# Kernel tuning notes

Measured on AMD Instinct MI355X. Metric: run time of the kernel, lower is better.

## Reference

```python
import jax, jax.numpy as jnp
import numpy as np

DIM, H, DH = 1024, 16, 64
SCALE = 1.0 / np.sqrt(DH)


def setup_inputs() -> dict:
    key = jax.random.key(0)
    ks = jax.random.split(key, 16)
    B, S = 2, 2048
    glorot = jax.nn.initializers.glorot_uniform()
    def qkv(k):
        return glorot(k, (DIM, H, DH), jnp.float32)
    inp = {
        "x": jax.random.normal(ks[0], (B, S, DIM), jnp.float32),
        "layer_idx": 3,
        "lambda_param": jnp.full((1,), 0.8, jnp.float32),
    }
    for i, br in enumerate(["1", "2"]):
        base = 1 + i * 4
        inp[f"Wq{br}"] = qkv(ks[base])
        inp[f"Wk{br}"] = qkv(ks[base + 1])
        inp[f"Wv{br}"] = qkv(ks[base + 2])
        inp[f"Wo{br}"] = glorot(ks[base + 3], (H, DH, DIM), jnp.float32).reshape(H, DH, DIM)
        inp[f"bq{br}"] = jnp.zeros((H, DH), jnp.float32)
        inp[f"bk{br}"] = jnp.zeros((H, DH), jnp.float32)
        inp[f"bv{br}"] = jnp.zeros((H, DH), jnp.float32)
        inp[f"bo{br}"] = jnp.zeros((DIM,), jnp.float32)
    inp["Wp"] = glorot(ks[9], (DIM, DIM), jnp.float32)
    inp["bp"] = jnp.zeros((DIM,), jnp.float32)
    return inp


def _mha(x, Wq, bq, Wk, bk, Wv, bv, Wo, bo):
    # x: [B,S,D]; per-head projections as in keras.layers.MultiHeadAttention
    q = jnp.einsum("bsd,dhk->bshk", x, Wq) + bq   # [B,S,H,Dh]
    k = jnp.einsum("bsd,dhk->bshk", x, Wk) + bk
    v = jnp.einsum("bsd,dhk->bshk", x, Wv) + bv
    scores = jnp.einsum("bqhd,bkhd->bhqk", q, k) * SCALE  # [B,H,S,S]
    attn = jax.nn.softmax(scores, axis=-1)
    o = jnp.einsum("bhqk,bkhd->bqhd", attn, v)            # [B,S,H,Dh]
    return jnp.einsum("bqhd,hdo->bqo", o, Wo) + bo        # [B,S,D]


def _get_lambda(lambda_param, layer_idx):
    lf = jnp.asarray(layer_idx, jnp.float32)
    exp_term = jnp.exp(-0.3 * jnp.maximum(lf - 1.0, 0.0))
    init = 0.8 - 0.6 * exp_term
    return jnp.clip(init * lambda_param[0], 0.1, 0.9)


def reference(x, layer_idx, lambda_param,
              Wq1, bq1, Wk1, bk1, Wv1, bv1, Wo1, bo1,
              Wq2, bq2, Wk2, bk2, Wv2, bv2, Wo2, bo2,
              Wp, bp):
    a1 = _mha(x, Wq1, bq1, Wk1, bk1, Wv1, bv1, Wo1, bo1)
    a2 = _mha(x, Wq2, bq2, Wk2, bk2, Wv2, bv2, Wo2, bo2)
    lam = _get_lambda(lambda_param, layer_idx)
    diff = a1 - lam * a2
    return diff @ Wp + bp  # dropout is identity at inference
```

## Files before the change

kernel.cpp:

```cpp
#include <hip/hip_runtime.h>
#include <math.h>

typedef unsigned short u16;
typedef __attribute__((ext_vector_type(8))) short bf16x8;
typedef __attribute__((ext_vector_type(4))) float f32x4;
typedef __attribute__((ext_vector_type(4))) unsigned short u16x4;
typedef __attribute__((ext_vector_type(8))) unsigned short u16x8;

constexpr int Sq = 2048, Dm = 1024, Hh = 16, DH = 64;
constexpr int NT = 4096;
constexpr float SEXP = 0.125f * 1.44269504f;

#if __has_builtin(__builtin_amdgcn_exp2f)
#define EXP2(x) __builtin_amdgcn_exp2f(x)
#else
#define EXP2(x) exp2f(x)
#endif

__device__ __forceinline__ u16 f2bf(float f) {
    unsigned u = __float_as_uint(f);
    return (u16)((u + 0x7FFF + ((u >> 16) & 1)) >> 16);
}

__device__ __forceinline__ void async16(u16* lds, const u16* g) {
    __builtin_amdgcn_global_load_lds(
        (const __attribute__((address_space(1))) unsigned int*)g,
        (__attribute__((address_space(3))) unsigned int*)lds, 16, 0, 0);
}

__device__ __forceinline__ float lam_of(const int* lidx, const float* lamp) {
    float lf = (float)lidx[0];
    float init = 0.8f - 0.6f * __expf(-0.3f * fmaxf(lf - 1.0f, 0.0f));
    return fminf(fmaxf(init * lamp[0], 0.1f), 0.9f);
}

__device__ __forceinline__ void gemm_tile_128(
    const u16* __restrict__ A, const u16* __restrict__ Bt, int K,
    int aRow0, int bCol0, u16* As, u16* Bs, f32x4 acc[4][4])
{
    const int tid = threadIdx.x;
    const int w = tid >> 6, lane = tid & 63;
    const int ln = lane & 15, quad = lane >> 4;
    const int wm = (w >> 1) * 64, wn = (w & 1) * 64;
    const int l3 = lane & 7, lr8 = lane >> 3;

    #pragma unroll
    for (int c0 = 0; c0 < 4; ++c0) {
        int c = w * 4 + c0;
        int lr = c * 8 + lr8;
        int sc = l3 ^ (lr & 7);
        async16(As + c * 512, A + (size_t)(aRow0 + lr) * K + sc * 8);
        async16(Bs + c * 512, Bt + (size_t)(bCol0 + lr) * K + sc * 8);
    }
    __syncthreads();

    int cur = 0;
    for (int kt = 0; kt < K; kt += 64) {
        const int ktn = kt + 64;
        if (ktn < K) {
            u16* Asn = As + (cur ^ 1) * 8192;
            u16* Bsn = Bs + (cur ^ 1) * 8192;
            #pragma unroll
            for (int c0 = 0; c0 < 4; ++c0) {
                int c = w * 4 + c0;
                int lr = c * 8 + lr8;
                int sc = l3 ^ (lr & 7);
                async16(Asn + c * 512, A + (size_t)(aRow0 + lr) * K + ktn + sc * 8);
                async16(Bsn + c * 512, Bt + (size_t)(bCol0 + lr) * K + ktn + sc * 8);
            }
        }
        const u16* Asc = As + cur * 8192;
        const u16* Bsc = Bs + cur * 8192;
        #pragma unroll
        for (int kc = 0; kc < 2; ++kc) {
            bf16x8 af[4], bfr[4];
            #pragma unroll
            for (int mt = 0; mt < 4; ++mt)
                af[mt] = *(const bf16x8*)(Asc + (wm + mt * 16 + ln) * 64 +
                                          (((kc * 4 + quad) ^ (ln & 7)) * 8));
            #pragma unroll
            for (int nt = 0; nt < 4; ++nt)
                bfr[nt] = *(const bf16x8*)(Bsc + (wn + nt * 16 + ln) * 64 +
                                           (((kc * 4 + quad) ^ (ln & 7)) * 8));
            #pragma unroll
            for (int mt = 0; mt < 4; ++mt)
                #pragma unroll
                for (int nt = 0; nt < 4; ++nt)
                    acc[mt][nt] = __builtin_amdgcn_mfma_f32_16x16x32_bf16(
                        af[mt], bfr[nt], acc[mt][nt], 0, 0, 0);
        }
        __syncthreads();
        cur ^= 1;
    }
}

__device__ __forceinline__ void gemm_tile_64(
    const u16* __restrict__ A, const u16* __restrict__ Bt, int K,
    int aRow0, int bCol0, u16* As, u16* Bs, f32x4 acc[2][4])
{
    const int tid = threadIdx.x;
    const int w = tid >> 6, lane = tid & 63;
    const int ln = lane & 15, quad = lane >> 4;
    const int wm = (w >> 1) * 32, wn = (w & 1) * 64;
    const int l3 = lane & 7, lr8 = lane >> 3;

    for (int kt = 0; kt < K; kt += 64) {
        __syncthreads();
        #pragma unroll
        for (int c0 = 0; c0 < 2; ++c0) {
            int c = w * 2 + c0;
            int lr = c * 8 + lr8;
            int sc = l3 ^ (lr & 7);
            async16(As + c * 512, A + (size_t)(aRow0 + lr) * K + kt + sc * 8);
        }
        #pragma unroll
        for (int c0 = 0; c0 < 4; ++c0) {
            int c = w * 4 + c0;
            int lr = c * 8 + lr8;
            int sc = l3 ^ (lr & 7);
            async16(Bs + c * 512, Bt + (size_t)(bCol0 + lr) * K + kt + sc * 8);
        }
        __syncthreads();
        #pragma unroll
        for (int kc = 0; kc < 2; ++kc) {
            bf16x8 af[2], bfr[4];
            #pragma unroll
            for (int mt = 0; mt < 2; ++mt)
                af[mt] = *(const bf16x8*)(As + (wm + mt * 16 + ln) * 64 +
                                          (((kc * 4 + quad) ^ (ln & 7)) * 8));
            #pragma unroll
            for (int nt = 0; nt < 4; ++nt)
                bfr[nt] = *(const bf16x8*)(Bs + (wn + nt * 16 + ln) * 64 +
                                           (((kc * 4 + quad) ^ (ln & 7)) * 8));
            #pragma unroll
            for (int mt = 0; mt < 2; ++mt)
                #pragma unroll
                for (int nt = 0; nt < 4; ++nt)
                    acc[mt][nt] = __builtin_amdgcn_mfma_f32_16x16x32_bf16(
                        af[mt], bfr[nt], acc[mt][nt], 0, 0, 0);
        }
    }
}

struct PrepP {
    const float* x; u16* xb;
    const float* wsrc[7]; u16* wdst[7];
    const float* Wo1; const float* Wo2;
    const float* bo1; const float* bo2;
    const int* lidx; const float* lamp;
    u16* Acat;
};

__global__ __launch_bounds__(256)
void prep(PrepP p)
{
    __shared__ float t[64][65];
    int b = blockIdx.x;
    const int tid = threadIdx.x;

    if (b < 4096) {
        int i = (b * 256 + tid) * 4;
        float4 v = *(const float4*)(p.x + i);
        u16x4 o;
        o.x = f2bf(v.x); o.y = f2bf(v.y); o.z = f2bf(v.z); o.w = f2bf(v.w);
        *(u16x4*)(p.xb + i) = o;
        return;
    }
    b -= 4096;
    if (b < 1792) {
        int z = b >> 8;
        int rem = b & 255;
        const float* __restrict__ src = p.wsrc[z];
        u16* __restrict__ dst = p.wdst[z];
        const int kb = (rem >> 4) * 64, nb = (rem & 15) * 64;
        {
            int r = tid >> 2, cs = (tid & 3) * 16;
            #pragma unroll
            for (int j4 = 0; j4 < 16; j4 += 4) {
                float4 v = *(const float4*)&src[(size_t)(kb + r) * 1024 + nb + cs + j4];
                t[r][cs + j4 + 0] = v.x; t[r][cs + j4 + 1] = v.y;
                t[r][cs + j4 + 2] = v.z; t[r][cs + j4 + 3] = v.w;
            }
        }
        __syncthreads();
        {
            int n = tid >> 2, ks = (tid & 3) * 16;
            u16x8 a2, b2;
            #pragma unroll
            for (int j = 0; j < 8; ++j) a2[j] = f2bf(t[ks + j][n]);
            #pragma unroll
            for (int j = 0; j < 8; ++j) b2[j] = f2bf(t[ks + 8 + j][n]);
            u16* o = &dst[(size_t)(nb + n) * 1024 + kb + ks];
            *(u16x8*)o = a2;
            *(u16x8*)(o + 8) = b2;
        }
        return;
    }
    b -= 1792;
    {
        const float lam = lam_of(p.lidx, p.lamp);
        int i = (b * 256 + tid) * 4;
        float4 v;
        if (i < 1048576) {
            v = *(const float4*)(p.Wo1 + i);
        } else if (i < 2097152) {
            v = *(const float4*)(p.Wo2 + (i - 1048576));
            v.x *= -lam; v.y *= -lam; v.z *= -lam; v.w *= -lam;
        } else {
            int c = i - 2097152;
            float4 a = *(const float4*)(p.bo1 + c);
            float4 b2 = *(const float4*)(p.bo2 + c);
            v.x = a.x - lam * b2.x; v.y = a.y - lam * b2.y;
            v.z = a.z - lam * b2.z; v.w = a.w - lam * b2.w;
        }
        u16x4 o;
        o.x = f2bf(v.x); o.y = f2bf(v.y); o.z = f2bf(v.z); o.w = f2bf(v.w);
        *(u16x4*)(p.Acat + i) = o;
    }
}

struct GemmP {
    const u16* xb;
    const u16* Wt[6]; const float* bias[6]; u16* out[6];
    const u16* Acat; const u16* Wpt; const float* bp;
    u16* Wfull_bt; float* bfull;
};

__global__ __launch_bounds__(256, 2)
void gemms(GemmP p)
{
    __shared__ u16 smem[32768];
    const int z = blockIdx.z;
    const int tid = threadIdx.x, w = tid >> 6, lane = tid & 63;
    const int ln = lane & 15, quad = lane >> 4;

    if (z == 6) {
        const int aRow0 = blockIdx.y * 64, nCol0 = blockIdx.x * 128;
        f32x4 acc[2][4] = {};
        gemm_tile_64(p.Acat, p.Wpt, 1024, aRow0, nCol0, smem, smem + 4096, acc);

        const int wm = (w >> 1) * 32, wn = (w & 1) * 64;
        #pragma unroll
        for (int mt = 0; mt < 2; ++mt) {
            #pragma unroll
            for (int nt = 0; nt < 4; ++nt) {
                int gn = nCol0 + wn + nt * 16 + ln;
                #pragma unroll
                for (int r = 0; r < 4; ++r) {
                    int gm = aRow0 + wm + mt * 16 + quad * 4 + r;
                    if (gm < 2048)
                        p.Wfull_bt[(size_t)gn * 2048 + gm] = f2bf(acc[mt][nt][r]);
                    else if (gm == 2048)
                        p.bfull[gn] = acc[mt][nt][r] + p.bp[gn];
                }
            }
        }
        return;
    }
    if (blockIdx.y >= 32) return;

    const int type = (z < 3) ? z : z - 3;
    const int aRow0 = blockIdx.y * 128, nCol0 = blockIdx.x * 128;
    f32x4 acc[4][4] = {};
    gemm_tile_128(p.xb, p.Wt[z], 1024, aRow0, nCol0, smem, smem + 16384, acc);

    const float* __restrict__ bias = p.bias[z];
    u16* __restrict__ out = p.out[z];
    const int wm = (w >> 1) * 64, wn = (w & 1) * 64;
    #pragma unroll
    for (int mt = 0; mt < 4; ++mt) {
        #pragma unroll
        for (int nt = 0; nt < 4; ++nt) {
            int gn = nCol0 + wn + nt * 16 + ln;
            int h = gn >> 6, dh = gn & 63;
            float bv = bias[gn];
            #pragma unroll
            for (int r = 0; r < 4; ++r) {
                int gm = aRow0 + wm + mt * 16 + quad * 4 + r;
                int b = gm >> 11, s = gm & (Sq - 1);
                size_t bh = (size_t)(b * Hh + h);
                float fv = acc[mt][nt][r] + bv;
                size_t idx;
                u16 val;
                if (type == 0) {
                    val = f2bf(fv * SEXP);
                    idx = bh * 131072 + (size_t)s * 64 + dh;
                } else if (type == 1) {
                    val = f2bf(fv);
                    idx = bh * 131072 + (size_t)(s >> 5) * 2048 +
                          (size_t)((dh >> 5) * 2 + ((s >> 4) & 1)) * 512 +
                          (size_t)(((dh >> 3) & 3) * 16 + (s & 15)) * 8 + (dh & 7);
                } else {
                    val = f2bf(fv);
                    int kidx = ((s & 15) * 2) + ((s >> 4) & 1);
                    idx = bh * 131072 + (size_t)(s >> 5) * 2048 +
                          (size_t)(dh >> 4) * 512 +
                          (size_t)((kidx >> 3) * 16 + (dh & 15)) * 8 + (kidx & 7);
                }
                out[idx] = val;
            }
        }
    }
}

__global__ __launch_bounds__(256, 4)
void attn_mfma(const u16* __restrict__ q1, const u16* __restrict__ kf1,
               const u16* __restrict__ vf1,
               const u16* __restrict__ q2, const u16* __restrict__ kf2,
               const u16* __restrict__ vf2, u16* __restrict__ ocat)
{
    __shared__ __align__(16) char smem[10240];

    const int bh = blockIdx.x, qblk = blockIdx.y, br = blockIdx.z;
    const u16* __restrict__ q  = br ? q2  : q1;
    const u16* __restrict__ kf = br ? kf2 : kf1;
    const u16* __restrict__ vf = br ? vf2 : vf1;

    const int tid = threadIdx.x, w = tid >> 6, lane = tid & 63;
    const int ln = lane & 15, quad = lane >> 4;
    char* Pbase = smem + w * 2560;

    const u16* qbase = q + (size_t)bh * 131072 +
                       (size_t)(qblk * 128 + w * 32) * 64;
    bf16x8 qf[2][2];
    #pragma unroll
    for (int mt = 0; mt < 2; ++mt)
        #pragma unroll
        for (int kc = 0; kc < 2; ++kc)
            qf[mt][kc] = *(const bf16x8*)(qbase + (mt * 16 + ln) * 64 +
                                          kc * 32 + quad * 8);

    bf16x8 ones;
    #pragma unroll
    for (int j = 0; j < 8; ++j) ones[j] = (short)0x3F80;
    const f32x4 zero4 = {0.f, 0.f, 0.f, 0.f};

    f32x4 oacc[2][4] = {};
    f32x4 lacc[2] = {};

    const u16* kbase = kf + (size_t)bh * 131072 + lane * 8;
    const u16* vbase = vf + (size_t)bh * 131072 + lane * 8;

    for (int it = 0; it < 32; ++it) {
        #pragma unroll
        for (int u = 0; u < 2; ++u) {
            const int kt = it * 2 + u;
            const u16* kp = kbase + (size_t)kt * 2048;
            const u16* vp = vbase + (size_t)kt * 2048;

            bf16x8 kfr[2][2];
            #pragma unroll
            for (int kc = 0; kc < 2; ++kc)
                #pragma unroll
                for (int nt = 0; nt < 2; ++nt)
                    kfr[nt][kc] = *(const bf16x8*)(kp + (kc * 2 + nt) * 512);

            __builtin_amdgcn_s_setprio(1);
            f32x4 sacc[2][2];
            #pragma unroll
            for (int mt = 0; mt < 2; ++mt)
                #pragma unroll
                for (int nt = 0; nt < 2; ++nt)
                    sacc[mt][nt] = __builtin_amdgcn_mfma_f32_16x16x32_bf16(
                        qf[mt][0], kfr[nt][0], zero4, 0, 0, 0);
            #pragma unroll
            for (int mt = 0; mt < 2; ++mt)
                #pragma unroll
                for (int nt = 0; nt < 2; ++nt)
                    sacc[mt][nt] = __builtin_amdgcn_mfma_f32_16x16x32_bf16(
                        qf[mt][1], kfr[nt][1], sacc[mt][nt], 0, 0, 0);
            __builtin_amdgcn_s_setprio(0);

            #pragma unroll
            for (int mt = 0; mt < 2; ++mt) {
                #pragma unroll
                for (int r = 0; r < 4; ++r) {
                    float p0 = EXP2(sacc[mt][0][r]);
                    float p1 = EXP2(sacc[mt][1][r]);
                    unsigned a  = __float_as_uint(p0) + 0x8000u;
                    unsigned b2 = __float_as_uint(p1) + 0x8000u;
                    unsigned pk = __builtin_amdgcn_perm(b2, a, 0x07060302);
                    int row = mt * 16 + quad * 4 + r;
                    *(unsigned*)(Pbase + row * 80 + (((ln >> 2) ^ r) << 4) +
                                 ((ln & 3) << 2)) = pk;
                }
            }

            bf16x8 vfr[4];
            #pragma unroll
            for (int dt = 0; dt < 4; ++dt)
                vfr[dt] = *(const bf16x8*)(vp + dt * 512);

            __builtin_amdgcn_s_setprio(1);
            #pragma unroll
            for (int mt = 0; mt < 2; ++mt) {
                bf16x8 pf = *(const bf16x8*)(Pbase + (mt * 16 + ln) * 80 +
                                             ((quad ^ (ln & 3)) << 4));
                lacc[mt] = __builtin_amdgcn_mfma_f32_16x16x32_bf16(
                    pf, ones, lacc[mt], 0, 0, 0);
                #pragma unroll
                for (int dt = 0; dt < 4; ++dt)
                    oacc[mt][dt] = __builtin_amdgcn_mfma_f32_16x16x32_bf16(
                        pf, vfr[dt], oacc[mt][dt], 0, 0, 0);
            }
            __builtin_amdgcn_s_setprio(0);
        }
        __builtin_amdgcn_s_barrier();
    }

    const int b = bh >> 4, h = bh & 15;
    #pragma unroll
    for (int mt = 0; mt < 2; ++mt) {
        #pragma unroll
        for (int r = 0; r < 4; ++r) {
            float inv = 1.0f / lacc[mt][r];
            int s = qblk * 128 + w * 32 + mt * 16 + quad * 4 + r;
            size_t rowb = (size_t)(b * Sq + s) * 2048 + br * 1024 + h * 64;
            #pragma unroll
            for (int dt = 0; dt < 4; ++dt)
                ocat[rowb + dt * 16 + ln] = f2bf(oacc[mt][dt][r] * inv);
        }
    }
}

__global__ __launch_bounds__(256, 4)
void out_mfma(const u16* __restrict__ ocat, const u16* __restrict__ Wfull_bt,
              const float* __restrict__ bfull, float* __restrict__ outb)
{
    __shared__ u16 As[64 * 64], Bs[128 * 64];
    const int aRow0 = blockIdx.y * 64, nCol0 = blockIdx.x * 128;
    f32x4 acc[2][4] = {};
    gemm_tile_64(ocat, Wfull_bt, 2048, aRow0, nCol0, As, Bs, acc);

    const int tid = threadIdx.x, w = tid >> 6, lane = tid & 63;
    const int ln = lane & 15, quad = lane >> 4;
    const int wm = (w >> 1) * 32, wn = (w & 1) * 64;
    #pragma unroll
    for (int mt = 0; mt < 2; ++mt) {
        #pragma unroll
        for (int nt = 0; nt < 4; ++nt) {
            int gn = nCol0 + wn + nt * 16 + ln;
            float bv = bfull[gn];
            #pragma unroll
            for (int r = 0; r < 4; ++r) {
                int gm = aRow0 + wm + mt * 16 + quad * 4 + r;
                outb[(size_t)gm * 1024 + gn] = acc[mt][nt][r] + bv;
            }
        }
    }
}

extern "C" void kernel_launch(void* const* d_in, const int* in_sizes, int n_in,
                              void* d_out, int out_size, void* d_ws, size_t ws_size,
                              hipStream_t stream)
{
    const float* x    = (const float*)d_in[0];
    const int*   lidx = (const int*)  d_in[1];
    const float* lamp = (const float*)d_in[2];
    const float* Wq1  = (const float*)d_in[3];
    const float* Wk1  = (const float*)d_in[4];
    const float* Wv1  = (const float*)d_in[5];
    const float* Wo1  = (const float*)d_in[6];
    const float* bq1  = (const float*)d_in[7];
    const float* bk1  = (const float*)d_in[8];
    const float* bv1  = (const float*)d_in[9];
    const float* bo1  = (const float*)d_in[10];
    const float* Wq2  = (const float*)d_in[11];
    const float* Wk2  = (const float*)d_in[12];
    const float* Wv2  = (const float*)d_in[13];
    const float* Wo2  = (const float*)d_in[14];
    const float* bq2  = (const float*)d_in[15];
    const float* bk2  = (const float*)d_in[16];
    const float* bv2  = (const float*)d_in[17];
    const float* bo2  = (const float*)d_in[18];
    const float* Wp   = (const float*)d_in[19];
    const float* bp   = (const float*)d_in[20];

    char* wsb = (char*)d_ws;
    const size_t MB = 1 << 20;
    u16* xb    = (u16*)(wsb + 0 * MB);
    u16* Wt0   = (u16*)(wsb + 8 * MB);
    u16* Wpt   = (u16*)(wsb + 20 * MB);
    u16* Acat  = (u16*)(wsb + 22 * MB);
    u16* Wfull = (u16*)(wsb + 27 * MB);
    float* bfull = (float*)(wsb + 31 * MB);
    u16* qb1   = (u16*)(wsb + 32 * MB);
    u16* kb1   = (u16*)(wsb + 40 * MB);
    u16* vb1   = (u16*)(wsb + 48 * MB);
    u16* qb2   = (u16*)(wsb + 56 * MB);
    u16* kb2   = (u16*)(wsb + 64 * MB);
    u16* vb2   = (u16*)(wsb + 72 * MB);
    u16* ocat  = (u16*)(wsb + 80 * MB);

    PrepP pp;
    pp.x = x; pp.xb = xb;
    const float* wsrc[7] = {Wq1, Wk1, Wv1, Wq2, Wk2, Wv2, Wp};
    for (int i = 0; i < 7; ++i) pp.wsrc[i] = wsrc[i];
    for (int i = 0; i < 6; ++i) pp.wdst[i] = Wt0 + (size_t)i * 1024 * 1024;
    pp.wdst[6] = Wpt;
    pp.Wo1 = Wo1; pp.Wo2 = Wo2; pp.bo1 = bo1; pp.bo2 = bo2;
    pp.lidx = lidx; pp.lamp = lamp; pp.Acat = Acat;
    prep<<<dim3(4096 + 1792 + 2049), dim3(256), 0, stream>>>(pp);

    GemmP gp;
    gp.xb = xb;
    gp.Wt[0] = Wt0 + 0 * 1048576; gp.bias[0] = bq1; gp.out[0] = qb1;
    gp.Wt[1] = Wt0 + 1 * 1048576; gp.bias[1] = bk1; gp.out[1] = kb1;
    gp.Wt[2] = Wt0 + 2 * 1048576; gp.bias[2] = bv1; gp.out[2] = vb1;
    gp.Wt[3] = Wt0 + 3 * 1048576; gp.bias[3] = bq2; gp.out[3] = qb2;
    gp.Wt[4] = Wt0 + 4 * 1048576; gp.bias[4] = bk2; gp.out[4] = kb2;
    gp.Wt[5] = Wt0 + 5 * 1048576; gp.bias[5] = bv2; gp.out[5] = vb2;
    gp.Acat = Acat; gp.Wpt = Wpt; gp.bp = bp;
    gp.Wfull_bt = Wfull; gp.bfull = bfull;
    gemms<<<dim3(8, 33, 7), dim3(256), 0, stream>>>(gp);

    attn_mfma<<<dim3(32, 16, 2), dim3(256), 0, stream>>>(
        qb1, kb1, vb1, qb2, kb2, vb2, ocat);

    out_mfma<<<dim3(8, 64), dim3(256), 0, stream>>>(
        ocat, Wfull, bfull, (float*)d_out);
}
```

Measured before the change: 318.6 us.

## Double-buffer 64-row GEMM tile and use partial vmcnt waits in both tiles

Turns gemm_tile_64 from a single-buffered load-then-compute loop into a double-buffered prefetch pipeline, matching gemm_tile_128. Both tiles now wait with partial s_waitcnt vmcnt counts plus raw barriers instead of full __syncthreads, so the next tile's global loads can stay in flight during MFMA compute. out_mfma doubles its LDS buffers and drops its occupancy hint from 4 to 3 blocks. The z==6 path offsets Bs to make room. The hand-written wait counts depend on the exact number of async loads issued per thread and may be fragile.

```diff
diff --git a/kernel.cpp b/kernel.cpp
--- a/kernel.cpp
+++ b/kernel.cpp
@@ -52,7 +52,6 @@
         async16(As + c * 512, A + (size_t)(aRow0 + lr) * K + sc * 8);
         async16(Bs + c * 512, Bt + (size_t)(bCol0 + lr) * K + sc * 8);
     }
-    __syncthreads();
 
     int cur = 0;
     for (int kt = 0; kt < K; kt += 64) {
@@ -68,7 +67,13 @@
                 async16(Asn + c * 512, A + (size_t)(aRow0 + lr) * K + ktn + sc * 8);
                 async16(Bsn + c * 512, Bt + (size_t)(bCol0 + lr) * K + ktn + sc * 8);
             }
-        }
+            asm volatile("s_waitcnt vmcnt(8)" ::: "memory");
+        } else {
+            asm volatile("s_waitcnt vmcnt(0)" ::: "memory");
+        }
+        __builtin_amdgcn_s_barrier();
+        __builtin_amdgcn_sched_barrier(0);
+
         const u16* Asc = As + cur * 8192;
         const u16* Bsc = Bs + cur * 8192;
         #pragma unroll
@@ -89,7 +94,9 @@
                     acc[mt][nt] = __builtin_amdgcn_mfma_f32_16x16x32_bf16(
                         af[mt], bfr[nt], acc[mt][nt], 0, 0, 0);
         }
-        __syncthreads();
+        asm volatile("s_waitcnt lgkmcnt(0)" ::: "memory");
+        __builtin_amdgcn_sched_barrier(0);
+        __builtin_amdgcn_s_barrier();
         cur ^= 1;
     }
 }
@@ -104,33 +111,60 @@
     const int wm = (w >> 1) * 32, wn = (w & 1) * 64;
     const int l3 = lane & 7, lr8 = lane >> 3;
 
+    #pragma unroll
+    for (int c0 = 0; c0 < 2; ++c0) {
+        int c = w * 2 + c0;
+        int lr = c * 8 + lr8;
+        int sc = l3 ^ (lr & 7);
+        async16(As + c * 512, A + (size_t)(aRow0 + lr) * K + sc * 8);
+    }
+    #pragma unroll
+    for (int c0 = 0; c0 < 4; ++c0) {
+        int c = w * 4 + c0;
+        int lr = c * 8 + lr8;
+        int sc = l3 ^ (lr & 7);
+        async16(Bs + c * 512, Bt + (size_t)(bCol0 + lr) * K + sc * 8);
+    }
+
+    int cur = 0;
     for (int kt = 0; kt < K; kt += 64) {
-        __syncthreads();
-        #pragma unroll
-        for (int c0 = 0; c0 < 2; ++c0) {
-            int c = w * 2 + c0;
-            int lr = c * 8 + lr8;
-            int sc = l3 ^ (lr & 7);
-            async16(As + c * 512, A + (size_t)(aRow0 + lr) * K + kt + sc * 8);
-        }
-        #pragma unroll
-        for (int c0 = 0; c0 < 4; ++c0) {
-            int c = w * 4 + c0;
-            int lr = c * 8 + lr8;
-            int sc = l3 ^ (lr & 7);
-            async16(Bs + c * 512, Bt + (size_t)(bCol0 + lr) * K + kt + sc * 8);
-        }
-        __syncthreads();
+        const int ktn = kt + 64;
+        if (ktn < K) {
+            u16* Asn = As + (cur ^ 1) * 4096;
+            u16* Bsn = Bs + (cur ^ 1) * 8192;
+            #pragma unroll
+            for (int c0 = 0; c0 < 2; ++c0) {
+                int c = w * 2 + c0;
+                int lr = c * 8 + lr8;
+                int sc = l3 ^ (lr & 7);
+                async16(Asn + c * 512, A + (size_t)(aRow0 + lr) * K + ktn + sc * 8);
+            }
+            #pragma unroll
+            for (int c0 = 0; c0 < 4; ++c0) {
+                int c = w * 4 + c0;
+                int lr = c * 8 + lr8;
+                int sc = l3 ^ (lr & 7);
+                async16(Bsn + c * 512, Bt + (size_t)(bCol0 + lr) * K + ktn + sc * 8);
+            }
+            asm volatile("s_waitcnt vmcnt(6)" ::: "memory");
+        } else {
+            asm volatile("s_waitcnt vmcnt(0)" ::: "memory");
+        }
+        __builtin_amdgcn_s_barrier();
+        __builtin_amdgcn_sched_barrier(0);
+
+        const u16* Asc = As + cur * 4096;
+        const u16* Bsc = Bs + cur * 8192;
         #pragma unroll
         for (int kc = 0; kc < 2; ++kc) {
             bf16x8 af[2], bfr[4];
             #pragma unroll
             for (int mt = 0; mt < 2; ++mt)
-                af[mt] = *(const bf16x8*)(As + (wm + mt * 16 + ln) * 64 +
+                af[mt] = *(const bf16x8*)(Asc + (wm + mt * 16 + ln) * 64 +
                                           (((kc * 4 + quad) ^ (ln & 7)) * 8));
             #pragma unroll
             for (int nt = 0; nt < 4; ++nt)
-                bfr[nt] = *(const bf16x8*)(Bs + (wn + nt * 16 + ln) * 64 +
+                bfr[nt] = *(const bf16x8*)(Bsc + (wn + nt * 16 + ln) * 64 +
                                            (((kc * 4 + quad) ^ (ln & 7)) * 8));
             #pragma unroll
             for (int mt = 0; mt < 2; ++mt)
@@ -139,6 +173,10 @@
                     acc[mt][nt] = __builtin_amdgcn_mfma_f32_16x16x32_bf16(
                         af[mt], bfr[nt], acc[mt][nt], 0, 0, 0);
         }
+        asm volatile("s_waitcnt lgkmcnt(0)" ::: "memory");
+        __builtin_amdgcn_sched_barrier(0);
+        __builtin_amdgcn_s_barrier();
+        cur ^= 1;
     }
 }
 
@@ -237,7 +275,7 @@
     if (z == 6) {
         const int aRow0 = blockIdx.y * 64, nCol0 = blockIdx.x * 128;
         f32x4 acc[2][4] = {};
-        gemm_tile_64(p.Acat, p.Wpt, 1024, aRow0, nCol0, smem, smem + 4096, acc);
+        gemm_tile_64(p.Acat, p.Wpt, 1024, aRow0, nCol0, smem, smem + 8192, acc);
 
         const int wm = (w >> 1) * 32, wn = (w & 1) * 64;
         #pragma unroll
@@ -423,11 +461,11 @@
     }
 }
 
-__global__ __launch_bounds__(256, 4)
+__global__ __launch_bounds__(256, 3)
 void out_mfma(const u16* __restrict__ ocat, const u16* __restrict__ Wfull_bt,
               const float* __restrict__ bfull, float* __restrict__ outb)
 {
-    __shared__ u16 As[64 * 64], Bs[128 * 64];
+    __shared__ u16 As[2 * 4096], Bs[2 * 8192];
     const int aRow0 = blockIdx.y * 64, nCol0 = blockIdx.x * 128;
     f32x4 acc[2][4] = {};
     gemm_tile_64(ocat, Wfull_bt, 2048, aRow0, nCol0, As, Bs, acc);
```

Measured after the change: 327.9 us. 1.03x slower.
